# Optimization experiments

Measured on AMD Instinct MI355X. Metric: run time of the kernel, lower is better.

The kernel has to match this reference:

```python
import jax, jax.numpy as jnp
import numpy as np
from jax import lax

SEQ_LEN, PRED_LEN, D_MODEL, ENC_IN, D_FF, N_LAYERS, N_HEADS = 336, 192, 512, 64, 2048, 2, 8
NUM_STEPS, COF, MARK, B, LABEL_LEN = 2, 0.1, 4, 32, 48


def _pos_emb(T, D):
    pos = np.arange(T)[:, None].astype(np.float32)
    div = np.exp(np.arange(0, D, 2).astype(np.float32) * (-np.log(10000.0) / D))
    pe = np.zeros((T, D), np.float32)
    pe[:, 0::2] = np.sin(pos * div)
    pe[:, 1::2] = np.cos(pos * div)
    return jnp.asarray(pe)


def _layer_norm(x, g, b):
    mu = x.mean(-1, keepdims=True)
    var = ((x - mu) ** 2).mean(-1, keepdims=True)
    return (x - mu) * lax.rsqrt(var + 1e-5) * g + b


def _embed(x, mark, conv_w, tf_w):
    # TokenEmbedding: circular Conv1d(kernel=3, pad=1) over time, no bias
    T = x.shape[1]
    xp = jnp.concatenate([x[:, -1:], x, x[:, :1]], axis=1)  # circular pad
    tok = sum(jnp.einsum('btc,cd->btd', xp[:, k:k + T], conv_w[k]) for k in range(3))
    return tok + _pos_emb(T, conv_w.shape[2])[None] + mark @ tf_w


def _block(x, p):
    Wq, Wk, Wv, Wo, bq, bk, bv, bo, g1, be1, W1, b1, W2, b2, g2, be2 = p
    Bb, T, D = x.shape
    dh = D // N_HEADS
    q = (x @ Wq + bq).reshape(Bb, T, N_HEADS, dh)
    k = (x @ Wk + bk).reshape(Bb, T, N_HEADS, dh)
    v = (x @ Wv + bv).reshape(Bb, T, N_HEADS, dh)
    att = jax.nn.softmax(jnp.einsum('bthd,bshd->bhts', q, k) / jnp.sqrt(jnp.float32(dh)), axis=-1)
    o = jnp.einsum('bhts,bshd->bthd', att, v).reshape(Bb, T, D) @ Wo + bo
    x = _layer_norm(x + o, g1, be1)
    ff = jax.nn.relu(x @ W1 + b1) @ W2 + b2
    return _layer_norm(x + ff, g2, be2)


def _gru(x, h, wih, whh, bih, bhh):
    gi = x @ wih.T + bih
    gh = h @ whh.T + bhh
    ir, iz, inn = jnp.split(gi, 3, axis=-1)
    hr, hz, hn = jnp.split(gh, 3, axis=-1)
    r = jax.nn.sigmoid(ir + hr)
    z = jax.nn.sigmoid(iz + hz)
    n = jnp.tanh(inn + r * hn)
    return (1.0 - z) * n + z * h


def _langevin(corrupt, cond, hx0, gru_p, score_w, alpha):
    # per-step GRU + energy-gradient update (Langevin refinement)
    def step(hx, xc):
        xi, ci = xc  # [B,C] each
        def energy(ri):
            h = _gru(jnp.concatenate([ri, ci], -1), hx, *gru_p)
            return (h @ score_w).sum() * COF, h
        g, h_new = jax.grad(energy, has_aux=True)(xi)
        return h_new, xi - alpha * g
    _, out = lax.scan(step, hx0, (corrupt.transpose(1, 0, 2), cond.transpose(1, 0, 2)))
    return out.transpose(1, 0, 2)  # [B,P,C]


def _forward(x_enc, x_mark_enc, batch_y, batch_y_mark, hx_init, token_conv_w, timefeat_w,
             Wq, Wk, Wv, Wo, bq, bk, bv, bo, ln1_g, ln1_b, W1, b1, W2, b2, ln2_g, ln2_b,
             pl1_w, pl1_b, pl2_w, pl2_b, proj_w, proj_b,
             gru_wih, gru_whh, gru_bih, gru_bhh, score_w, alpha):
    means = lax.stop_gradient(x_enc.mean(1, keepdims=True))
    xe = x_enc - means
    stdev = jnp.sqrt(xe.var(1, keepdims=True) + 1e-5)  # not detached in torch code
    xe = xe / stdev
    # predict_linear1 over time axis: [B,T,C] -> [B,P,C]
    pre = jnp.einsum('btc,pt->bpc', xe, pl1_w) + pl1_b[None, :, None]
    ymark = batch_y_mark[:, -PRED_LEN:, :]
    gru_p = (gru_wih, gru_whh, gru_bih, gru_bhh)
    local_loss = jnp.float32(0.0)
    out_dn = None
    for s in range(NUM_STEPS):
        corrupt = lax.stop_gradient(pre)
        corrupt = jnp.einsum('bpc,qp->bqc', corrupt, pl2_w) + pl2_b[None, :, None]
        emb = _embed(corrupt, ymark, token_conv_w, timefeat_w)
        for l in range(N_LAYERS):
            emb = _block(emb, (Wq[l], Wk[l], Wv[l], Wo[l], bq[l], bk[l], bv[l], bo[l],
                               ln1_g[l], ln1_b[l], W1[l], b1[l], W2[l], b2[l], ln2_g[l], ln2_b[l]))
        cond = emb @ proj_w.T + proj_b
        out = _langevin(corrupt, cond, hx_init[s], gru_p, score_w, alpha)
        pre = out
        out_dn = out * stdev[:, 0, :][:, None, :] + means[:, 0, :][:, None, :]
        local_loss = local_loss + jnp.mean(jnp.abs(out_dn - batch_y[:, -PRED_LEN:, :]))
    return out_dn, local_loss


def setup_inputs() -> dict:
    key = jax.random.key(0)
    ks = iter(jax.random.split(key, 64))
    r = lambda shape, s=0.02: jax.random.normal(next(ks), shape, dtype=jnp.float32) * s
    inp = dict(
        x_enc=jax.random.normal(next(ks), (B, SEQ_LEN, ENC_IN), dtype=jnp.float32),
        x_mark_enc=jax.random.normal(next(ks), (B, SEQ_LEN, MARK), dtype=jnp.float32),
        batch_y=jax.random.normal(next(ks), (B, LABEL_LEN + PRED_LEN, ENC_IN), dtype=jnp.float32),
        batch_y_mark=jax.random.normal(next(ks), (B, LABEL_LEN + PRED_LEN, MARK), dtype=jnp.float32),
        hx_init=jax.random.normal(next(ks), (NUM_STEPS, B, D_MODEL), dtype=jnp.float32),
        token_conv_w=r((3, ENC_IN, D_MODEL)),
        timefeat_w=r((MARK, D_MODEL)),
        Wq=r((N_LAYERS, D_MODEL, D_MODEL)), Wk=r((N_LAYERS, D_MODEL, D_MODEL)),
        Wv=r((N_LAYERS, D_MODEL, D_MODEL)), Wo=r((N_LAYERS, D_MODEL, D_MODEL)),
        bq=jnp.zeros((N_LAYERS, D_MODEL)), bk=jnp.zeros((N_LAYERS, D_MODEL)),
        bv=jnp.zeros((N_LAYERS, D_MODEL)), bo=jnp.zeros((N_LAYERS, D_MODEL)),
        ln1_g=jnp.ones((N_LAYERS, D_MODEL)), ln1_b=jnp.zeros((N_LAYERS, D_MODEL)),
        W1=r((N_LAYERS, D_MODEL, D_FF)), b1=jnp.zeros((N_LAYERS, D_FF)),
        W2=r((N_LAYERS, D_FF, D_MODEL)), b2=jnp.zeros((N_LAYERS, D_MODEL)),
        ln2_g=jnp.ones((N_LAYERS, D_MODEL)), ln2_b=jnp.zeros((N_LAYERS, D_MODEL)),
        pl1_w=r((PRED_LEN, SEQ_LEN), 0.05), pl1_b=jnp.zeros((PRED_LEN,)),
        pl2_w=r((PRED_LEN, PRED_LEN), 0.05), pl2_b=jnp.zeros((PRED_LEN,)),
        proj_w=r((ENC_IN, D_MODEL)), proj_b=jnp.zeros((ENC_IN,)),
        gru_wih=r((3 * D_MODEL, 2 * ENC_IN), 0.04), gru_whh=r((3 * D_MODEL, D_MODEL), 0.04),
        gru_bih=jnp.zeros((3 * D_MODEL,)), gru_bhh=jnp.zeros((3 * D_MODEL,)),
        score_w=r((D_MODEL,), 0.04),
        alpha=jnp.array([0.1], dtype=jnp.float32),
    )
    return inp


def reference(x_enc, x_mark_enc, batch_y, batch_y_mark, hx_init, token_conv_w, timefeat_w,
              Wq, Wk, Wv, Wo, bq, bk, bv, bo, ln1_g, ln1_b, W1, b1, W2, b2, ln2_g, ln2_b,
              pl1_w, pl1_b, pl2_w, pl2_b, proj_w, proj_b,
              gru_wih, gru_whh, gru_bih, gru_bhh, score_w, alpha):
    out, loss = _forward(x_enc, x_mark_enc, batch_y, batch_y_mark, hx_init, token_conv_w, timefeat_w,
                         Wq, Wk, Wv, Wo, bq, bk, bv, bo, ln1_g, ln1_b, W1, b1, W2, b2, ln2_g, ln2_b,
                         pl1_w, pl1_b, pl2_w, pl2_b, proj_w, proj_b,
                         gru_wih, gru_whh, gru_bih, gru_bhh, score_w, alpha)
    return out[:, -PRED_LEN:, :], loss
```

## Files before the change

### kernel.cpp

```cpp
#include <hip/hip_runtime.h>
#include <math.h>

#define BATCH 32
#define TT    192
#define DM    512
#define CIN   64
#define SEQL  336
#define DFF   2048
#define NH    8
#define COF   0.1f
#define OUTN  (BATCH*TT*CIN)

typedef _Float16 h2_t __attribute__((ext_vector_type(2)));
union H2U { unsigned int u; h2_t h; };

typedef short bf16x8 __attribute__((ext_vector_type(8)));
typedef float f32x4 __attribute__((ext_vector_type(4)));
typedef unsigned int u32x4 __attribute__((ext_vector_type(4)));

__device__ __forceinline__ unsigned short f2bf(float v) {
  union { float f; unsigned int u; } a; a.f = v;
  unsigned int r = (a.u + 0x7fffu + ((a.u >> 16) & 1u)) >> 16;
  return (unsigned short)r;
}

__device__ __forceinline__ void gload16(const unsigned short* g, unsigned short* l) {
  __builtin_amdgcn_global_load_lds(
      (const __attribute__((address_space(1))) void*)g,
      (__attribute__((address_space(3))) void*)l, 16, 0, 0);
}

__device__ __forceinline__ int sd4(unsigned int a, unsigned int b, int c) {
#if __has_builtin(__builtin_amdgcn_sdot4)
  return __builtin_amdgcn_sdot4((int)a, (int)b, c, false);
#else
  c += (int)(signed char)(a & 0xff) * (int)(signed char)(b & 0xff);
  c += (int)(signed char)((a >> 8) & 0xff) * (int)(signed char)((b >> 8) & 0xff);
  c += (int)(signed char)((a >> 16) & 0xff) * (int)(signed char)((b >> 16) & 0xff);
  c += (int)(signed char)(a >> 24) * (int)(signed char)(b >> 24);
  return c;
#endif
}

__device__ __forceinline__ int sd16(u32x4 w, u32x4 h, int acc) {
  acc = sd4(w[0], h[0], acc); acc = sd4(w[1], h[1], acc);
  acc = sd4(w[2], h[2], acc); acc = sd4(w[3], h[3], acc);
  return acc;
}

__device__ __forceinline__ unsigned int packq4(const float* hp) {
  int a = (int)rintf(hp[0] * 15.875f); a = a < -127 ? -127 : (a > 127 ? 127 : a);
  int b = (int)rintf(hp[1] * 15.875f); b = b < -127 ? -127 : (b > 127 ? 127 : b);
  int c = (int)rintf(hp[2] * 15.875f); c = c < -127 ? -127 : (c > 127 ? 127 : c);
  int d = (int)rintf(hp[3] * 15.875f); d = d < -127 ? -127 : (d > 127 ? 127 : d);
  return (unsigned int)((a & 0xff) | ((b & 0xff) << 8) | ((c & 0xff) << 16) |
                        ((d & 0xff) << 24));
}


__global__ void zero_loss_kernel(float* loss) {
  if (threadIdx.x == 0) loss[0] = 0.f;
}

__global__ void zero_hqg_kernel(unsigned long long* p) {
  p[blockIdx.x * 256 + threadIdx.x] = 0ull;
}

__global__ void finalize_kernel(float* dout, const float* loss) {
  dout[OUTN] = loss[0] * (1.f / (float)OUTN);
}

__global__ void pe_table_kernel(float* __restrict__ peT) {
  int t = blockIdx.x, d = threadIdx.x;
  int i2 = (d >> 1) * 2;
  float freq = expf((float)i2 * (-9.210340371976184f / (float)DM));
  float ang = (float)t * freq;
  peT[(size_t)t * DM + d] = (d & 1) ? cosf(ang) : sinf(ang);
}

__global__ void stats_kernel(const float* __restrict__ x, float* __restrict__ means,
                             float* __restrict__ stdev) {
  int b = blockIdx.x, c = threadIdx.x;
  const float* xb = x + (size_t)b * SEQL * CIN + c;
  float s = 0.f;
  for (int t = 0; t < SEQL; t++) s += xb[t * CIN];
  float mu = s * (1.f / SEQL);
  float s2 = 0.f;
  for (int t = 0; t < SEQL; t++) { float d = xb[t * CIN] - mu; s2 += d * d; }
  means[b * CIN + c] = mu;
  stdev[b * CIN + c] = sqrtf(s2 * (1.f / SEQL) + 1e-5f);
}

__global__ void pl1_kernel(const float* __restrict__ x, const float* __restrict__ means,
                           const float* __restrict__ stdev, const float* __restrict__ w,
                           const float* __restrict__ bias, float* __restrict__ pre) {
  int p = blockIdx.x, b = blockIdx.y, c = threadIdx.x;
  float mu = means[b * CIN + c];
  float inv = 1.f / stdev[b * CIN + c];
  const float* xb = x + (size_t)b * SEQL * CIN + c;
  const float* wp = w + p * SEQL;
  float acc = 0.f;
  for (int t = 0; t < SEQL; t++) acc += (xb[t * CIN] - mu) * wp[t];
  pre[((size_t)b * TT + p) * CIN + c] = acc * inv + bias[p];
}

__global__ void pl2_kernel(const float* __restrict__ pre, const float* __restrict__ w,
                           const float* __restrict__ bias, float* __restrict__ out,
                           unsigned short* __restrict__ xc) {
  int q = blockIdx.x, b = blockIdx.y, c = threadIdx.x;
  const float* pb = pre + (size_t)b * TT * CIN + c;
  const float* wq = w + q * TT;
  float acc = 0.f;
  for (int p = 0; p < TT; p++) acc += pb[p * CIN] * wq[p];
  float val = acc + bias[q];
  size_t r = (size_t)b * TT + q;
  out[r * CIN + c] = val;
  xc[r * 128 + c] = f2bf(val);
}

__global__ void embed_kernel(const float* __restrict__ corrupt, const float* __restrict__ ymark,
                             const float* __restrict__ conv_w, const float* __restrict__ tf_w,
                             const float* __restrict__ peT, float* __restrict__ emb,
                             unsigned short* __restrict__ embB) {
  int t = blockIdx.x, b = blockIdx.y, d = threadIdx.x;
  __shared__ float xm[CIN], x0[CIN], xp[CIN], mk[4];
  int tm = (t + TT - 1) % TT, tp = (t + 1) % TT;
  if (d < CIN) {
    xm[d] = corrupt[((size_t)b * TT + tm) * CIN + d];
    x0[d] = corrupt[((size_t)b * TT + t) * CIN + d];
    xp[d] = corrupt[((size_t)b * TT + tp) * CIN + d];
  }
  if (d < 4) mk[d] = ymark[((size_t)b * 240 + 48 + t) * 4 + d];
  __syncthreads();
  float acc = 0.f;
  const float* w0 = conv_w + d;
  const float* w1 = conv_w + CIN * DM + d;
  const float* w2 = conv_w + 2 * CIN * DM + d;
  #pragma unroll 8
  for (int c = 0; c < CIN; c++)
    acc += xm[c] * w0[c * DM] + x0[c] * w1[c * DM] + xp[c] * w2[c * DM];
  float pe = peT[(size_t)t * DM + d];
  float mkacc = mk[0] * tf_w[d] + mk[1] * tf_w[DM + d] + mk[2] * tf_w[2 * DM + d] +
                mk[3] * tf_w[3 * DM + d];
  float val = acc + pe + mkacc;
  size_t o = ((size_t)b * TT + t) * DM + d;
  emb[o] = val;
  embB[o] = f2bf(val);
}

template <int TB, int RELU, int XC>
__global__ __launch_bounds__(256) void gemm_kernel(const float* __restrict__ A,
                                                   const float* __restrict__ B,
                                                   const float* __restrict__ bias,
                                                   float* __restrict__ C,
                                                   unsigned short* __restrict__ Cx,
                                                   int M, int N, int K) {
  __shared__ float As[16][68];
  __shared__ float Bs[16][68];
  int tid = threadIdx.x;
  int bn = blockIdx.x * 64, bm = blockIdx.y * 64;
  int tx = tid & 15, ty = tid >> 4;
  int row0 = ty * 4, col0 = tx * 4;
  float acc[4][4] = {};
  for (int k0 = 0; k0 < K; k0 += 16) {
    {
      int m = tid >> 2, kq = (tid & 3) << 2;
      float4 av = *(const float4*)&A[(size_t)(bm + m) * K + k0 + kq];
      As[kq + 0][m] = av.x; As[kq + 1][m] = av.y; As[kq + 2][m] = av.z; As[kq + 3][m] = av.w;
    }
    if (TB) {
      int n = tid >> 2, kq = (tid & 3) << 2;
      float4 bv = *(const float4*)&B[(size_t)(bn + n) * K + k0 + kq];
      Bs[kq + 0][n] = bv.x; Bs[kq + 1][n] = bv.y; Bs[kq + 2][n] = bv.z; Bs[kq + 3][n] = bv.w;
    } else {
      int kk = tid >> 4, nq = (tid & 15) << 2;
      float4 bv = *(const float4*)&B[(size_t)(k0 + kk) * N + bn + nq];
      *(float4*)&Bs[kk][nq] = bv;
    }
    __syncthreads();
    #pragma unroll
    for (int k = 0; k < 16; k++) {
      float4 a4 = *(const float4*)&As[k][row0];
      float4 b4 = *(const float4*)&Bs[k][col0];
      float a[4] = {a4.x, a4.y, a4.z, a4.w};
      float bb[4] = {b4.x, b4.y, b4.z, b4.w};
      #pragma unroll
      for (int i = 0; i < 4; i++)
        #pragma unroll
        for (int j = 0; j < 4; j++) acc[i][j] += a[i] * bb[j];
    }
    __syncthreads();
  }
  float bv[4] = {0.f, 0.f, 0.f, 0.f};
  if (bias) *(float4*)bv = *(const float4*)&bias[bn + col0];
  #pragma unroll
  for (int i = 0; i < 4; i++) {
    float ov[4];
    #pragma unroll
    for (int j = 0; j < 4; j++) {
      float v = acc[i][j] + bv[j];
      if (RELU) v = fmaxf(v, 0.f);
      ov[j] = v;
    }
    if (XC) {
      unsigned short xv[4];
      #pragma unroll
      for (int j = 0; j < 4; j++) xv[j] = f2bf(ov[j]);
      *(uint2*)&Cx[(size_t)(bm + row0 + i) * 128 + 64 + bn + col0] = *(uint2*)xv;
    } else {
      *(float4*)&C[(size_t)(bm + row0 + i) * N + bn + col0] = *(float4*)ov;
    }
  }
}

template <int RELU, int WF32, int WBF16>
__global__ __launch_bounds__(256) void gemm_bf16_kernel(
    const unsigned short* __restrict__ A, const unsigned short* __restrict__ Bt,
    const float* __restrict__ bias, float* __restrict__ C, unsigned short* __restrict__ Cb,
    int M, int N, int K) {
  __shared__ __align__(16) unsigned short As[128 * 32];
  __shared__ __align__(16) unsigned short Bs[128 * 32];
  int tid = threadIdx.x;
  int bm = blockIdx.y * 128, bn = blockIdx.x * 128;
  int wave = tid >> 6, lane = tid & 63;
  int wm = (wave >> 1) * 64, wn = (wave & 1) * 64;
  int r15 = lane & 15, q = lane >> 4;
  f32x4 acc[4][4] = {};
  int srow = wave * 32 + (lane >> 2);
  int scol = (lane & 3) * 8;
  for (int k0 = 0; k0 < K; k0 += 32) {
    gload16(&A[(size_t)(bm + srow) * K + k0 + scol], &As[(wave * 32) * 32]);
    gload16(&A[(size_t)(bm + srow + 16) * K + k0 + scol], &As[(wave * 32 + 16) * 32]);
    gload16(&Bt[(size_t)(bn + srow) * K + k0 + scol], &Bs[(wave * 32) * 32]);
    gload16(&Bt[(size_t)(bn + srow + 16) * K + k0 + scol], &Bs[(wave * 32 + 16) * 32]);
    __syncthreads();
    bf16x8 af[4], bfr[4];
    #pragma unroll
    for (int mi = 0; mi < 4; mi++)
      af[mi] = *(const bf16x8*)&As[(wm + mi * 16 + r15) * 32 + q * 8];
    #pragma unroll
    for (int ni = 0; ni < 4; ni++)
      bfr[ni] = *(const bf16x8*)&Bs[(wn + ni * 16 + r15) * 32 + q * 8];
    #pragma unroll
    for (int mi = 0; mi < 4; mi++)
      #pragma unroll
      for (int ni = 0; ni < 4; ni++)
        acc[mi][ni] =
            __builtin_amdgcn_mfma_f32_16x16x32_bf16(af[mi], bfr[ni], acc[mi][ni], 0, 0, 0);
    __syncthreads();
  }
  #pragma unroll
  for (int mi = 0; mi < 4; mi++) {
    #pragma unroll
    for (int ni = 0; ni < 4; ni++) {
      int col = bn + wn + ni * 16 + r15;
      float bv = bias ? bias[col] : 0.f;
      #pragma unroll
      for (int v = 0; v < 4; v++) {
        int row = bm + wm + mi * 16 + q * 4 + v;
        float val = acc[mi][ni][v] + bv;
        if (RELU) val = fmaxf(val, 0.f);
        if (WF32) C[(size_t)row * N + col] = val;
        if (WBF16) Cb[(size_t)row * N + col] = f2bf(val);
      }
    }
  }
}

__global__ __launch_bounds__(256) void axpy_partial_kernel(
    const unsigned short* __restrict__ A, const unsigned short* __restrict__ Bt,
    float* __restrict__ P, int M, int K) {
  __shared__ __align__(16) unsigned short As[128 * 32];
  __shared__ __align__(16) unsigned short Bs[128 * 32];
  int tid = threadIdx.x;
  int kq = blockIdx.x;
  int bm = blockIdx.y * 128;
  int wave = tid >> 6, lane = tid & 63;
  int wm = (wave >> 1) * 64, wn = (wave & 1) * 64;
  int r15 = lane & 15, q = lane >> 4;
  f32x4 acc[4][4] = {};
  int srow = wave * 32 + (lane >> 2);
  int scol = (lane & 3) * 8;
  int kbeg = kq * (K >> 2), kend = (kq + 1) * (K >> 2);
  for (int k0 = kbeg; k0 < kend; k0 += 32) {
    gload16(&A[(size_t)(bm + srow) * K + k0 + scol], &As[(wave * 32) * 32]);
    gload16(&A[(size_t)(bm + srow + 16) * K + k0 + scol], &As[(wave * 32 + 16) * 32]);
    gload16(&Bt[(size_t)srow * K + k0 + scol], &Bs[(wave * 32) * 32]);
    gload16(&Bt[(size_t)(srow + 16) * K + k0 + scol], &Bs[(wave * 32 + 16) * 32]);
    __syncthreads();
    bf16x8 af[4], bfr[4];
    #pragma unroll
    for (int mi = 0; mi < 4; mi++)
      af[mi] = *(const bf16x8*)&As[(wm + mi * 16 + r15) * 32 + q * 8];
    #pragma unroll
    for (int ni = 0; ni < 4; ni++)
      bfr[ni] = *(const bf16x8*)&Bs[(wn + ni * 16 + r15) * 32 + q * 8];
    #pragma unroll
    for (int mi = 0; mi < 4; mi++)
      #pragma unroll
      for (int ni = 0; ni < 4; ni++)
        acc[mi][ni] =
            __builtin_amdgcn_mfma_f32_16x16x32_bf16(af[mi], bfr[ni], acc[mi][ni], 0, 0, 0);
    __syncthreads();
  }
  #pragma unroll
  for (int mi = 0; mi < 4; mi++) {
    #pragma unroll
    for (int ni = 0; ni < 4; ni++) {
      int col = wn + ni * 16 + r15;
      if (col < 64) {
        #pragma unroll
        for (int v = 0; v < 4; v++) {
          int row = bm + wm + mi * 16 + q * 4 + v;
          P[(size_t)kq * OUTN + (size_t)row * 64 + col] = acc[mi][ni][v];
        }
      }
    }
  }
}

__global__ __launch_bounds__(256) void pack_transpose_bf16_kernel(
    const float* __restrict__ src, unsigned short* __restrict__ dst, int K, int N) {
  __shared__ unsigned short tile[64][65];
  int kb = blockIdx.x * 64, nb = blockIdx.y * 64;
  int tid = threadIdx.x;
  int tn = tid & 63, tk = tid >> 6;
  #pragma unroll
  for (int i = 0; i < 16; i++) {
    int k = tk + i * 4;
    tile[k][tn] = f2bf(src[(size_t)(kb + k) * N + nb + tn]);
  }
  __syncthreads();
  int tk2 = tid & 63, tn2 = tid >> 6;
  #pragma unroll
  for (int i = 0; i < 16; i++) {
    int n = tn2 + i * 4;
    dst[(size_t)(nb + n) * K + kb + tk2] = tile[tk2][n];
  }
}

__global__ void pack_bf16_kernel(const float* __restrict__ src, unsigned short* __restrict__ dst,
                                 int n) {
  int idx = blockIdx.x * 256 + threadIdx.x;
  if (idx < n) dst[idx] = f2bf(src[idx]);
}

__global__ void pack_wxproj_kernel(const float* __restrict__ wih,
                                   unsigned short* __restrict__ dst) {
  int idx = blockIdx.x * 256 + threadIdx.x;
  int k = idx % 1536, n = idx / 1536;
  float v = (n < 64) ? wih[(size_t)k * 128 + n] : 0.f;
  dst[idx] = f2bf(v);
}

__global__ void concat_qkv_bias_kernel(const float* __restrict__ bq, const float* __restrict__ bk,
                                       const float* __restrict__ bv, float* __restrict__ dst) {
  int l = blockIdx.y;
  int i = blockIdx.x * 256 + threadIdx.x;
  float v = (i < 512) ? bq[l * 512 + i]
                      : ((i < 1024) ? bk[l * 512 + i - 512] : bv[l * 512 + i - 1024]);
  dst[l * 1536 + i] = v;
}

__global__ __launch_bounds__(256) void attention_mfma_kernel(
    const unsigned short* __restrict__ qkv, unsigned short* __restrict__ attnO) {
  __shared__ __align__(16) unsigned short Ks[192 * 72];
  __shared__ __align__(16) unsigned short Vt[64 * 200];
  __shared__ __align__(16) float Ps[4][16 * 36];
  int h = blockIdx.x, b = blockIdx.y;
  int tid = threadIdx.x, wave = tid >> 6, lane = tid & 63;
  int m = lane & 15, q = lane >> 4;
  const unsigned short* Qg = qkv + (size_t)b * TT * 1536 + h * 64;
  const unsigned short* Kg = Qg + 512;
  const unsigned short* Vg = Qg + 1024;
  for (int idx = tid; idx < 192 * 8; idx += 256) {
    int s = idx >> 3, ch = (idx & 7) * 8;
    *(uint4*)&Ks[s * 72 + ch] = *(const uint4*)&Kg[(size_t)s * 1536 + ch];
  }
  for (int idx = tid; idx < 96 * 8; idx += 256) {
    int sp = idx >> 3, co = (idx & 7) * 8;
    uint4 v0 = *(const uint4*)&Vg[(size_t)(2 * sp) * 1536 + co];
    uint4 v1 = *(const uint4*)&Vg[(size_t)(2 * sp + 1) * 1536 + co];
    const unsigned short* e0 = (const unsigned short*)&v0;
    const unsigned short* e1 = (const unsigned short*)&v1;
    unsigned int* vtw = (unsigned int*)Vt;
    #pragma unroll
    for (int u = 0; u < 8; u++)
      vtw[(co + u) * 100 + sp] = (unsigned int)e0[u] | ((unsigned int)e1[u] << 16);
  }
  __syncthreads();
  float* ps = Ps[wave];
  for (int tile = wave; tile < 12; tile += 4) {
    int t0 = tile * 16;
    bf16x8 qf0 = *(const bf16x8*)&Qg[(size_t)(t0 + m) * 1536 + q * 8];
    bf16x8 qf1 = *(const bf16x8*)&Qg[(size_t)(t0 + m) * 1536 + 32 + q * 8];
    f32x4 S[12];
    #pragma unroll
    for (int nt = 0; nt < 12; nt++) {
      bf16x8 kf0 = *(const bf16x8*)&Ks[(nt * 16 + m) * 72 + q * 8];
      bf16x8 kf1 = *(const bf16x8*)&Ks[(nt * 16 + m) * 72 + 32 + q * 8];
      f32x4 a = {0.f, 0.f, 0.f, 0.f};
      a = __builtin_amdgcn_mfma_f32_16x16x32_bf16(qf0, kf0, a, 0, 0, 0);
      a = __builtin_amdgcn_mfma_f32_16x16x32_bf16(qf1, kf1, a, 0, 0, 0);
      S[nt] = a;
    }
    float mx[4] = {-1e30f, -1e30f, -1e30f, -1e30f};
    #pragma unroll
    for (int nt = 0; nt < 12; nt++)
      #pragma unroll
      for (int v = 0; v < 4; v++) {
        S[nt][v] *= 0.125f;
        mx[v] = fmaxf(mx[v], S[nt][v]);
      }
    #pragma unroll
    for (int d = 1; d < 16; d <<= 1) {
      #pragma unroll
      for (int v = 0; v < 4; v++) mx[v] = fmaxf(mx[v], __shfl_xor(mx[v], d));
    }
    float sm[4] = {0.f, 0.f, 0.f, 0.f};
    #pragma unroll
    for (int nt = 0; nt < 12; nt++)
      #pragma unroll
      for (int v = 0; v < 4; v++) {
        float e = __expf(S[nt][v] - mx[v]);
        S[nt][v] = e;
        sm[v] += e;
      }
    #pragma unroll
    for (int d = 1; d < 16; d <<= 1) {
      #pragma unroll
      for (int v = 0; v < 4; v++) sm[v] += __shfl_xor(sm[v], d);
    }
    float inv[4];
    #pragma unroll
    for (int v = 0; v < 4; v++) inv[v] = 1.f / sm[v];
    f32x4 o[4] = {};
    for (int kc = 0; kc < 6; kc++) {
      asm volatile("s_waitcnt lgkmcnt(0)" ::: "memory");
      #pragma unroll
      for (int half = 0; half < 2; half++) {
        int nt = 2 * kc + half;
        #pragma unroll
        for (int v = 0; v < 4; v++) ps[(q * 4 + v) * 36 + half * 16 + m] = S[nt][v];
      }
      asm volatile("s_waitcnt lgkmcnt(0)" ::: "memory");
      float4 p0 = *(const float4*)&ps[m * 36 + q * 8];
      float4 p1 = *(const float4*)&ps[m * 36 + q * 8 + 4];
      unsigned short tmp[8];
      tmp[0] = f2bf(p0.x); tmp[1] = f2bf(p0.y); tmp[2] = f2bf(p0.z); tmp[3] = f2bf(p0.w);
      tmp[4] = f2bf(p1.x); tmp[5] = f2bf(p1.y); tmp[6] = f2bf(p1.z); tmp[7] = f2bf(p1.w);
      bf16x8 pf = *(bf16x8*)tmp;
      #pragma unroll
      for (int nt2 = 0; nt2 < 4; nt2++) {
        bf16x8 vf = *(const bf16x8*)&Vt[(nt2 * 16 + m) * 200 + kc * 32 + q * 8];
        o[nt2] = __builtin_amdgcn_mfma_f32_16x16x32_bf16(pf, vf, o[nt2], 0, 0, 0);
      }
    }
    #pragma unroll
    for (int nt2 = 0; nt2 < 4; nt2++)
      #pragma unroll
      for (int v = 0; v < 4; v++) {
        size_t row = (size_t)b * TT + t0 + q * 4 + v;
        attnO[row * 512 + h * 64 + nt2 * 16 + m] = f2bf(o[nt2][v] * inv[v]);
      }
  }
}

__global__ __launch_bounds__(256) void ln_residual_kernel(float* __restrict__ x,
                                                          const float* __restrict__ res,
                                                          const float* __restrict__ g,
                                                          const float* __restrict__ b,
                                                          unsigned short* __restrict__ xb) {
  int row = blockIdx.x, tid = threadIdx.x;
  __shared__ float red[256];
  float* xr = x + (size_t)row * DM;
  const float* rr = res + (size_t)row * DM;
  float v0 = xr[tid] + rr[tid];
  float v1 = xr[tid + 256] + rr[tid + 256];
  red[tid] = v0 + v1;
  __syncthreads();
  if (tid < 128) red[tid] += red[tid + 128];
  __syncthreads();
  if (tid < 64) red[tid] += red[tid + 64];
  __syncthreads();
  float rv = red[tid & 63];
  #pragma unroll
  for (int s = 32; s > 0; s >>= 1) rv += __shfl_down(rv, s);
  float mu = __shfl(rv, 0) * (1.f / DM);
  __syncthreads();
  float d0 = v0 - mu, d1 = v1 - mu;
  red[tid] = d0 * d0 + d1 * d1;
  __syncthreads();
  if (tid < 128) red[tid] += red[tid + 128];
  __syncthreads();
  if (tid < 64) red[tid] += red[tid + 64];
  __syncthreads();
  rv = red[tid & 63];
  #pragma unroll
  for (int s = 32; s > 0; s >>= 1) rv += __shfl_down(rv, s);
  float rstd = rsqrtf(__shfl(rv, 0) * (1.f / DM) + 1e-5f);
  float o0 = d0 * rstd * g[tid] + b[tid];
  float o1 = d1 * rstd * g[tid + 256] + b[tid + 256];
  xr[tid] = o0;
  xr[tid + 256] = o1;
  xb[(size_t)row * DM + tid] = f2bf(o0);
  xb[(size_t)row * DM + tid + 256] = f2bf(o1);
}

__global__ void pack_whh_q8_kernel(const float* __restrict__ whh, signed char* __restrict__ whhJ,
                                   float* __restrict__ sws) {
  int row = blockIdx.x;
  int lane = threadIdx.x;
  const float* src = whh + (size_t)row * 512;
  float mx = 0.f;
  for (int k = lane; k < 512; k += 64) mx = fmaxf(mx, fabsf(src[k]));
  for (int off = 32; off > 0; off >>= 1) mx = fmaxf(mx, __shfl_xor(mx, off));
  float inv = (mx > 0.f) ? 127.f / mx : 0.f;
  if (lane == 0) sws[row] = (mx / 127.f) * (8.f / 127.f);
  int g = row >> 9, jj = row & 511;
  int quad = jj >> 7, jl = jj & 127;
  for (int k = lane; k < 512; k += 64) {
    int qv = (int)rintf(src[k] * inv);
    qv = qv < -127 ? -127 : (qv > 127 ? 127 : qv);
    int kh = k >> 6, u = (k >> 4) & 3, m = k & 15;
    whhJ[((size_t)(((quad * 128 + jl) * 8 + kh) * 4 + u) * 3 + g) * 16 + m] = (signed char)qv;
  }
}

__global__ __launch_bounds__(1024, 4) void langevin_scan_kernel(
    const float* __restrict__ gi_all, const float* __restrict__ hx0,
    const signed char* __restrict__ whhJ, const float* __restrict__ sws,
    const float* __restrict__ bhh, const float* __restrict__ score_w,
    unsigned short* __restrict__ dgiB, unsigned long long* __restrict__ hqg, int tagBase) {
  int b = blockIdx.x, quad = blockIdx.y;
  int tid = threadIdx.x;
  __shared__ __align__(16) unsigned int hqp[2][160];
  int jl = tid >> 3, kh = tid & 7;
  int j = quad * 128 + jl;
  bool act = (kh == 0);
  float bhr = 0.f, bhz = 0.f, bhn = 0.f, sw = 0.f, swr = 0.f, swz = 0.f, swn = 0.f, h = 0.f;
  if (act) {
    bhr = bhh[j]; bhz = bhh[512 + j]; bhn = bhh[1024 + j];
    sw = score_w[j] * COF;
    swr = sws[j]; swz = sws[512 + j]; swn = sws[1024 + j];
    h = hx0[(size_t)b * 512 + j];
  }
  if (tid < 128) {
    float4 hv = *(const float4*)&hx0[(size_t)b * 512 + tid * 4];
    float tmp[4] = {hv.x, hv.y, hv.z, hv.w};
    hqp[0][(tid >> 4) * 20 + (tid & 15)] = packq4(tmp);
  }
  const u32x4* wbase = (const u32x4*)whhJ + (size_t)((quad * 128 + jl) * 8 + kh) * 12;
  u32x4 wreg[12];
  #pragma unroll
  for (int i = 0; i < 12; i++) wreg[i] = wbase[i];
  #pragma unroll
  for (int i = 0; i < 12; i++) asm volatile("" : "+v"(wreg[i]));
  float gir = 0.f, giz = 0.f, gin = 0.f, gir1 = 0.f, giz1 = 0.f, gin1 = 0.f;
  if (act) {
    const float* g0 = &gi_all[(size_t)b * TT * 1536];
    gir = g0[j]; giz = g0[512 + j]; gin = g0[1024 + j];
    const float* g1 = g0 + 1536;
    gir1 = g1[j]; giz1 = g1[512 + j]; gin1 = g1[1024 + j];
  }
  __syncthreads();
  for (int t = 0; t < TT; t++) {
    int rb = t & 1;
    int ir = 0, iz = 0, in_ = 0;
    #pragma unroll
    for (int u = 0; u < 4; u++) {
      u32x4 hqv = *(const u32x4*)&hqp[rb][kh * 20 + u * 4];
      ir = sd16(wreg[u * 3 + 0], hqv, ir);
      iz = sd16(wreg[u * 3 + 1], hqv, iz);
      in_ = sd16(wreg[u * 3 + 2], hqv, in_);
    }
    #pragma unroll
    for (int d = 1; d < 8; d <<= 1) {
      ir += __shfl_xor(ir, d);
      iz += __shfl_xor(iz, d);
      in_ += __shfl_xor(in_, d);
    }
    int qv = 0;
    float r = 0.f, z = 0.f, n = 0.f, hnv = 0.f, hj = 0.f;
    if (act) {
      float gr = (float)ir * swr, gz = (float)iz * swz, gn2 = (float)in_ * swn;
      r = 1.f / (1.f + expf(-(gir + gr + bhr)));
      z = 1.f / (1.f + expf(-(giz + gz + bhz)));
      hnv = gn2 + bhn;
      n = tanhf(gin + r * hnv);
      hj = h;
      h = (1.f - z) * n + z * hj;
      int q = (int)rintf(h * 15.875f);
      qv = q < -127 ? -127 : (q > 127 ? 127 : q);
    }
    int l = tid & 63;
    int q1 = __shfl(qv, (l + 8) & 63);
    int q2 = __shfl(qv, (l + 16) & 63);
    int q3 = __shfl(qv, (l + 24) & 63);
    bool ex = (t + 1 < TT);
    int wb = (t + 1) & 1;
    unsigned tag = (unsigned)(tagBase + t + 1);
    if (ex && (tid & 31) == 0) {
      unsigned word = (unsigned)(qv & 0xff) | ((unsigned)(q1 & 0xff) << 8) |
                      ((unsigned)(q2 & 0xff) << 16) | ((unsigned)(q3 & 0xff) << 24);
      int w = quad * 32 + (tid >> 5);
      hqp[wb][(w >> 4) * 20 + (w & 15)] = word;
      __hip_atomic_store(&hqg[((size_t)wb * BATCH + b) * 128 + w],
                         ((unsigned long long)tag << 32) | (unsigned long long)word,
                         __ATOMIC_RELAXED, __HIP_MEMORY_SCOPE_AGENT);
    }
    float dg0 = 0.f, dg1 = 0.f, dg2 = 0.f;
    if (act) {
      float dinn = sw * (1.f - z) * (1.f - n * n);
      dg0 = dinn * hnv * r * (1.f - r);
      dg1 = sw * (hj - n) * z * (1.f - z);
      dg2 = dinn;
    }
    if (ex && kh == 1 && jl < 96) {
      int o = jl >> 5;
      int oq = (quad + 1 + o) & 3;
      int w = oq * 32 + (jl & 31);
      unsigned long long* p = &hqg[((size_t)wb * BATCH + b) * 128 + w];
      unsigned long long v = __hip_atomic_load(p, __ATOMIC_RELAXED, __HIP_MEMORY_SCOPE_AGENT);
      while ((unsigned)(v >> 32) != tag) {
        __builtin_amdgcn_s_sleep(1);
        v = __hip_atomic_load(p, __ATOMIC_RELAXED, __HIP_MEMORY_SCOPE_AGENT);
      }
      hqp[wb][(w >> 4) * 20 + (w & 15)] = (unsigned)v;
    }
    __builtin_amdgcn_sched_barrier(0);
    float girP = 0.f, gizP = 0.f, ginP = 0.f;
    if (act && t + 2 < TT) {
      const float* gp = &gi_all[((size_t)b * TT + t + 2) * 1536];
      girP = gp[j]; gizP = gp[512 + j]; ginP = gp[1024 + j];
    }
    if (act) {
      size_t drow = ((size_t)b * TT + t) * 1536;
      dgiB[drow + j] = f2bf(dg0);
      dgiB[drow + 512 + j] = f2bf(dg1);
      dgiB[drow + 1024 + j] = f2bf(dg2);
    }
    if (ex) __syncthreads();
    gir = gir1; giz = giz1; gin = gin1;
    gir1 = girP; giz1 = gizP; gin1 = ginP;
  }
}

__global__ __launch_bounds__(256) void denorm_loss_fused_kernel(
    const float* __restrict__ P, const float* __restrict__ R,
    const float* __restrict__ alphaPtr, const float* __restrict__ stdev,
    const float* __restrict__ means, const float* __restrict__ y,
    float* __restrict__ outn, float* __restrict__ dout, float* __restrict__ loss) {
  int idx = blockIdx.x * 256 + threadIdx.x;
  int tid = threadIdx.x;
  int c = idx & 63;
  int bt = idx >> 6;
  int t = bt % TT, b = bt / TT;
  float al = alphaPtr[0];
  float val = P[idx] + P[OUTN + idx] + P[2 * (size_t)OUTN + idx] + P[3 * (size_t)OUTN + idx];
  float on = R[idx] - al * val;
  outn[idx] = on;
  float od = on * stdev[b * CIN + c] + means[b * CIN + c];
  dout[idx] = od;
  float diff = fabsf(od - y[((size_t)b * 240 + 48 + t) * CIN + c]);
  __shared__ float red[256];
  red[tid] = diff;
  __syncthreads();
  if (tid < 128) red[tid] += red[tid + 128];
  __syncthreads();
  if (tid < 64) red[tid] += red[tid + 64];
  __syncthreads();
  if (tid < 64) {
    float rv = red[tid];
    #pragma unroll
    for (int s = 32; s > 0; s >>= 1) rv += __shfl_down(rv, s);
    if (tid == 0) atomicAdd(loss, rv);
  }
}

extern "C" void kernel_launch(void* const* d_in, const int* in_sizes, int n_in, void* d_out,
                              int out_size, void* d_ws, size_t ws_size, hipStream_t stream) {
  const float* x_enc = (const float*)d_in[0];
  const float* batch_y = (const float*)d_in[2];
  const float* y_mark = (const float*)d_in[3];
  const float* hx_init = (const float*)d_in[4];
  const float* conv_w = (const float*)d_in[5];
  const float* tf_w = (const float*)d_in[6];
  const float* Wq = (const float*)d_in[7];
  const float* Wk = (const float*)d_in[8];
  const float* Wv = (const float*)d_in[9];
  const float* Wo = (const float*)d_in[10];
  const float* bq = (const float*)d_in[11];
  const float* bk = (const float*)d_in[12];
  const float* bv = (const float*)d_in[13];
  const float* bo = (const float*)d_in[14];
  const float* ln1_g = (const float*)d_in[15];
  const float* ln1_b = (const float*)d_in[16];
  const float* W1 = (const float*)d_in[17];
  const float* b1 = (const float*)d_in[18];
  const float* W2 = (const float*)d_in[19];
  const float* b2 = (const float*)d_in[20];
  const float* ln2_g = (const float*)d_in[21];
  const float* ln2_b = (const float*)d_in[22];
  const float* pl1_w = (const float*)d_in[23];
  const float* pl1_b = (const float*)d_in[24];
  const float* pl2_w = (const float*)d_in[25];
  const float* pl2_b = (const float*)d_in[26];
  const float* proj_w = (const float*)d_in[27];
  const float* proj_b = (const float*)d_in[28];
  const float* gru_wih = (const float*)d_in[29];
  const float* gru_whh = (const float*)d_in[30];
  const float* gru_bih = (const float*)d_in[31];
  const float* gru_bhh = (const float*)d_in[32];
  const float* score_w = (const float*)d_in[33];
  const float* alpha = (const float*)d_in[34];
  float* dout = (float*)d_out;

  float* W = (float*)d_ws;
  size_t off = 0;
  float* means = W + off;   off += 2048;
  float* stdev = W + off;   off += 2048;
  float* lossacc = W + off; off += 64;
  float* preA = W + off;    off += (size_t)OUTN;
  float* outA = W + off;    off += (size_t)OUTN;
  float* outB = W + off;    off += (size_t)OUTN;
  float* corrupt = W + off; off += (size_t)OUTN;
  float* peT = W + off;     off += (size_t)TT * DM;
  float* axp = W + off;     off += (size_t)4 * OUTN;
  signed char* whhJ = (signed char*)(W + off); off += 786432 / 4;
  float* sws = W + off;     off += 1536;
  unsigned long long* hqg = (unsigned long long*)(W + off); off += 2 * BATCH * 128 * 2;
  float* emb = W + off;     off += (size_t)BATCH * TT * DM;
  float* Kb = W + off;      off += (size_t)BATCH * TT * DM;
  float* gi_all = W + off;  off += (size_t)BATCH * TT * 1536;
  unsigned short* embB = (unsigned short*)(W + off);  off += (size_t)BATCH * TT * DM / 2;
  unsigned short* qkvB = (unsigned short*)(W + off);  off += (size_t)BATCH * TT * 1536 / 2;
  unsigned short* attnOB = (unsigned short*)(W + off); off += (size_t)BATCH * TT * DM / 2;
  unsigned short* FFbB = (unsigned short*)(W + off);  off += (size_t)BATCH * TT * DFF / 2;
  unsigned short* xcatB = (unsigned short*)(W + off); off += (size_t)BATCH * TT * 128 / 2;
  float* bqkv = W + off;    off += 2 * 1536;
  unsigned short* WxProjB = (unsigned short*)(W + off); off += (size_t)128 * 1536 / 2;
  unsigned short* wT = (unsigned short*)(W + off);
  const size_t SQ = (size_t)DM * DM;
  const size_t SFF = (size_t)DM * DFF;
  const size_t LAYER = 4 * SQ + 2 * SFF;
  unsigned short* wihB = wT + 2 * LAYER;
  off += (2 * LAYER + (size_t)1536 * 128) / 2 + 64;
  unsigned short* dgiB = qkvB;

  const int M = BATCH * TT;

  zero_loss_kernel<<<1, 64, 0, stream>>>(lossacc);
  zero_hqg_kernel<<<32, 256, 0, stream>>>(hqg);
  pe_table_kernel<<<TT, DM, 0, stream>>>(peT);
  stats_kernel<<<BATCH, 64, 0, stream>>>(x_enc, means, stdev);
  pl1_kernel<<<dim3(TT, BATCH), 64, 0, stream>>>(x_enc, means, stdev, pl1_w, pl1_b, preA);
  pack_whh_q8_kernel<<<1536, 64, 0, stream>>>(gru_whh, whhJ, sws);
  pack_wxproj_kernel<<<(128 * 1536) / 256, 256, 0, stream>>>(gru_wih, WxProjB);
  concat_qkv_bias_kernel<<<dim3(6, 2), 256, 0, stream>>>(bq, bk, bv, bqkv);
  for (int l = 0; l < 2; l++) {
    unsigned short* base = wT + (size_t)l * LAYER;
    pack_transpose_bf16_kernel<<<dim3(8, 8), 256, 0, stream>>>(Wq + (size_t)l * SQ, base, DM, DM);
    pack_transpose_bf16_kernel<<<dim3(8, 8), 256, 0, stream>>>(Wk + (size_t)l * SQ, base + SQ, DM, DM);
    pack_transpose_bf16_kernel<<<dim3(8, 8), 256, 0, stream>>>(Wv + (size_t)l * SQ, base + 2 * SQ, DM, DM);
    pack_transpose_bf16_kernel<<<dim3(8, 8), 256, 0, stream>>>(Wo + (size_t)l * SQ, base + 3 * SQ, DM, DM);
    pack_transpose_bf16_kernel<<<dim3(8, 32), 256, 0, stream>>>(W1 + (size_t)l * SFF, base + 4 * SQ, DM, DFF);
    pack_transpose_bf16_kernel<<<dim3(32, 8), 256, 0, stream>>>(W2 + (size_t)l * SFF, base + 4 * SQ + SFF, DFF, DM);
  }
  pack_bf16_kernel<<<(1536 * 128) / 256, 256, 0, stream>>>(gru_wih, wihB, 1536 * 128);

  const float* pre = preA;
  float* outs[2] = {outA, outB};
  for (int s = 0; s < 2; s++) {
    pl2_kernel<<<dim3(TT, BATCH), 64, 0, stream>>>(pre, pl2_w, pl2_b, corrupt, xcatB);
    embed_kernel<<<dim3(TT, BATCH), DM, 0, stream>>>(corrupt, y_mark, conv_w, tf_w, peT, emb,
                                                     embB);
    for (int l = 0; l < 2; l++) {
      unsigned short* base = wT + (size_t)l * LAYER;
      gemm_bf16_kernel<0, 0, 1><<<dim3(1536 / 128, M / 128), 256, 0, stream>>>(
          embB, base, bqkv + l * 1536, nullptr, qkvB, M, 1536, DM);
      attention_mfma_kernel<<<dim3(NH, BATCH), 256, 0, stream>>>(qkvB, attnOB);
      gemm_bf16_kernel<0, 1, 0><<<dim3(DM / 128, M / 128), 256, 0, stream>>>(
          attnOB, base + 3 * SQ, bo + l * DM, Kb, nullptr, M, DM, DM);
      ln_residual_kernel<<<M, 256, 0, stream>>>(emb, Kb, ln1_g + l * DM, ln1_b + l * DM, embB);
      gemm_bf16_kernel<1, 0, 1><<<dim3(DFF / 128, M / 128), 256, 0, stream>>>(
          embB, base + 4 * SQ, b1 + l * DFF, nullptr, FFbB, M, DFF, DM);
      gemm_bf16_kernel<0, 1, 0><<<dim3(DM / 128, M / 128), 256, 0, stream>>>(
          FFbB, base + 4 * SQ + SFF, b2 + l * DM, Kb, nullptr, M, DM, DFF);
      ln_residual_kernel<<<M, 256, 0, stream>>>(emb, Kb, ln2_g + l * DM, ln2_b + l * DM, embB);
    }
    gemm_kernel<1, 0, 1><<<dim3(CIN / 64, M / 64), 256, 0, stream>>>(
        emb, proj_w, proj_b, nullptr, xcatB, M, CIN, DM);
    gemm_bf16_kernel<0, 1, 0><<<dim3(1536 / 128, M / 128), 256, 0, stream>>>(
        xcatB, wihB, gru_bih, gi_all, nullptr, M, 1536, 128);
    langevin_scan_kernel<<<dim3(BATCH, 4), 1024, 0, stream>>>(
        gi_all, hx_init + (size_t)s * BATCH * DM, whhJ, sws, gru_bhh, score_w, dgiB, hqg,
        s * TT);
    axpy_partial_kernel<<<dim3(4, M / 128), 256, 0, stream>>>(dgiB, WxProjB, axp, M, 1536);
    denorm_loss_fused_kernel<<<OUTN / 256, 256, 0, stream>>>(
        axp, corrupt, alpha, stdev, means, batch_y, outs[s], dout, lossacc);
    pre = outs[s];
  }
  finalize_kernel<<<1, 1, 0, stream>>>(dout, lossacc);
}
```

Measured before the change: 2.360 ms.

## Recast token and time-feature embedding as a tiled GEMM over an im2col buffer

Replaces the per-(t,b) embed kernel, which rereads the conv and time-feature weights from global memory for every token, with an im2col-style build of a padded [M,208] input matrix followed by the existing tiled fp32 GEMM against a stacked weight matrix. The positional encoding is added and the bf16 copy written in the GEMM epilogue. This adds an extra kernel launch and a round trip of the Xp buffer through memory, but gives shared-memory weight reuse across rows. The embedding stage is a small part of the total runtime.

```diff
diff --git a/kernel.cpp b/kernel.cpp
--- a/kernel.cpp
+++ b/kernel.cpp
@@ -10,6 +10,7 @@
 #define NH    8
 #define COF   0.1f
 #define OUTN  (BATCH*TT*CIN)
+#define KEMB  208
 
 typedef _Float16 h2_t __attribute__((ext_vector_type(2)));
 union H2U { unsigned int u; h2_t h; };
@@ -76,6 +77,38 @@
   float freq = expf((float)i2 * (-9.210340371976184f / (float)DM));
   float ang = (float)t * freq;
   peT[(size_t)t * DM + d] = (d & 1) ? cosf(ang) : sinf(ang);
+}
+
+__global__ void build_wemb_kernel(const float* __restrict__ conv_w,
+                                  const float* __restrict__ tf_w, float* __restrict__ Wemb) {
+  int idx = blockIdx.x * 256 + threadIdx.x;
+  int n = idx % DM, k = idx / DM;
+  float v = 0.f;
+  if (k < 192) v = conv_w[(size_t)k * DM + n];
+  else if (k < 196) v = tf_w[(size_t)(k - 192) * DM + n];
+  Wemb[idx] = v;
+}
+
+__global__ void build_xp_kernel(const float* __restrict__ corrupt,
+                                const float* __restrict__ ymark, float* __restrict__ Xp) {
+  int idx = blockIdx.x * 256 + threadIdx.x;
+  int col = idx % KEMB, row = idx / KEMB;
+  int b = row / TT, t = row % TT;
+  float v;
+  if (col < 64) {
+    int tm = (t + TT - 1) % TT;
+    v = corrupt[((size_t)b * TT + tm) * CIN + col];
+  } else if (col < 128) {
+    v = corrupt[((size_t)b * TT + t) * CIN + (col - 64)];
+  } else if (col < 192) {
+    int tp = (t + 1) % TT;
+    v = corrupt[((size_t)b * TT + tp) * CIN + (col - 128)];
+  } else if (col < 196) {
+    v = ymark[((size_t)b * 240 + 48 + t) * 4 + (col - 192)];
+  } else {
+    v = 0.f;
+  }
+  Xp[idx] = v;
 }
 
 __global__ void stats_kernel(const float* __restrict__ x, float* __restrict__ means,
@@ -118,42 +151,14 @@
   xc[r * 128 + c] = f2bf(val);
 }
 
-__global__ void embed_kernel(const float* __restrict__ corrupt, const float* __restrict__ ymark,
-                             const float* __restrict__ conv_w, const float* __restrict__ tf_w,
-                             const float* __restrict__ peT, float* __restrict__ emb,
-                             unsigned short* __restrict__ embB) {
-  int t = blockIdx.x, b = blockIdx.y, d = threadIdx.x;
-  __shared__ float xm[CIN], x0[CIN], xp[CIN], mk[4];
-  int tm = (t + TT - 1) % TT, tp = (t + 1) % TT;
-  if (d < CIN) {
-    xm[d] = corrupt[((size_t)b * TT + tm) * CIN + d];
-    x0[d] = corrupt[((size_t)b * TT + t) * CIN + d];
-    xp[d] = corrupt[((size_t)b * TT + tp) * CIN + d];
-  }
-  if (d < 4) mk[d] = ymark[((size_t)b * 240 + 48 + t) * 4 + d];
-  __syncthreads();
-  float acc = 0.f;
-  const float* w0 = conv_w + d;
-  const float* w1 = conv_w + CIN * DM + d;
-  const float* w2 = conv_w + 2 * CIN * DM + d;
-  #pragma unroll 8
-  for (int c = 0; c < CIN; c++)
-    acc += xm[c] * w0[c * DM] + x0[c] * w1[c * DM] + xp[c] * w2[c * DM];
-  float pe = peT[(size_t)t * DM + d];
-  float mkacc = mk[0] * tf_w[d] + mk[1] * tf_w[DM + d] + mk[2] * tf_w[2 * DM + d] +
-                mk[3] * tf_w[3 * DM + d];
-  float val = acc + pe + mkacc;
-  size_t o = ((size_t)b * TT + t) * DM + d;
-  emb[o] = val;
-  embB[o] = f2bf(val);
-}
-
-template <int TB, int RELU, int XC>
+template <int TB, int RELU, int XC, int EMB>
 __global__ __launch_bounds__(256) void gemm_kernel(const float* __restrict__ A,
                                                    const float* __restrict__ B,
                                                    const float* __restrict__ bias,
                                                    float* __restrict__ C,
                                                    unsigned short* __restrict__ Cx,
+                                                   const float* __restrict__ PE,
+                                                   unsigned short* __restrict__ Cb2,
                                                    int M, int N, int K) {
   __shared__ float As[16][68];
   __shared__ float Bs[16][68];
@@ -195,10 +200,17 @@
   if (bias) *(float4*)bv = *(const float4*)&bias[bn + col0];
   #pragma unroll
   for (int i = 0; i < 4; i++) {
+    int row = bm + row0 + i;
+    float pe[4] = {0.f, 0.f, 0.f, 0.f};
+    if (EMB) {
+      int t = row % TT;
+      *(float4*)pe = *(const float4*)&PE[(size_t)t * DM + bn + col0];
+    }
     float ov[4];
     #pragma unroll
     for (int j = 0; j < 4; j++) {
       float v = acc[i][j] + bv[j];
+      if (EMB) v += pe[j];
       if (RELU) v = fmaxf(v, 0.f);
       ov[j] = v;
     }
@@ -206,9 +218,15 @@
       unsigned short xv[4];
       #pragma unroll
       for (int j = 0; j < 4; j++) xv[j] = f2bf(ov[j]);
-      *(uint2*)&Cx[(size_t)(bm + row0 + i) * 128 + 64 + bn + col0] = *(uint2*)xv;
+      *(uint2*)&Cx[(size_t)row * 128 + 64 + bn + col0] = *(uint2*)xv;
     } else {
-      *(float4*)&C[(size_t)(bm + row0 + i) * N + bn + col0] = *(float4*)ov;
+      *(float4*)&C[(size_t)row * N + bn + col0] = *(float4*)ov;
+      if (EMB) {
+        unsigned short xv[4];
+        #pragma unroll
+        for (int j = 0; j < 4; j++) xv[j] = f2bf(ov[j]);
+        *(uint2*)&Cb2[(size_t)row * N + bn + col0] = *(uint2*)xv;
+      }
     }
   }
 }
@@ -726,7 +744,9 @@
   float* outB = W + off;    off += (size_t)OUTN;
   float* corrupt = W + off; off += (size_t)OUTN;
   float* peT = W + off;     off += (size_t)TT * DM;
+  float* Wemb = W + off;    off += (size_t)KEMB * DM;
   float* axp = W + off;     off += (size_t)4 * OUTN;
+  float* Xp = axp;
   signed char* whhJ = (signed char*)(W + off); off += 786432 / 4;
   float* sws = W + off;     off += 1536;
   unsigned long long* hqg = (unsigned long long*)(W + off); off += 2 * BATCH * 128 * 2;
@@ -753,6 +773,7 @@
   zero_loss_kernel<<<1, 64, 0, stream>>>(lossacc);
   zero_hqg_kernel<<<32, 256, 0, stream>>>(hqg);
   pe_table_kernel<<<TT, DM, 0, stream>>>(peT);
+  build_wemb_kernel<<<(KEMB * DM) / 256, 256, 0, stream>>>(conv_w, tf_w, Wemb);
   stats_kernel<<<BATCH, 64, 0, stream>>>(x_enc, means, stdev);
   pl1_kernel<<<dim3(TT, BATCH), 64, 0, stream>>>(x_enc, means, stdev, pl1_w, pl1_b, preA);
   pack_whh_q8_kernel<<<1536, 64, 0, stream>>>(gru_whh, whhJ, sws);
@@ -773,8 +794,9 @@
   float* outs[2] = {outA, outB};
   for (int s = 0; s < 2; s++) {
     pl2_kernel<<<dim3(TT, BATCH), 64, 0, stream>>>(pre, pl2_w, pl2_b, corrupt, xcatB);
-    embed_kernel<<<dim3(TT, BATCH), DM, 0, stream>>>(corrupt, y_mark, conv_w, tf_w, peT, emb,
-                                                     embB);
+    build_xp_kernel<<<(M * KEMB) / 256, 256, 0, stream>>>(corrupt, y_mark, Xp);
+    gemm_kernel<0, 0, 0, 1><<<dim3(DM / 64, M / 64), 256, 0, stream>>>(
+        Xp, Wemb, nullptr, emb, nullptr, peT, embB, M, DM, KEMB);
     for (int l = 0; l < 2; l++) {
       unsigned short* base = wT + (size_t)l * LAYER;
       gemm_bf16_kernel<0, 0, 1><<<dim3(1536 / 128, M / 128), 256, 0, stream>>>(
@@ -789,8 +811,8 @@
           FFbB, base + 4 * SQ + SFF, b2 + l * DM, Kb, nullptr, M, DM, DFF);
       ln_residual_kernel<<<M, 256, 0, stream>>>(emb, Kb, ln2_g + l * DM, ln2_b + l * DM, embB);
     }
-    gemm_kernel<1, 0, 1><<<dim3(CIN / 64, M / 64), 256, 0, stream>>>(
-        emb, proj_w, proj_b, nullptr, xcatB, M, CIN, DM);
+    gemm_kernel<1, 0, 1, 0><<<dim3(CIN / 64, M / 64), 256, 0, stream>>>(
+        emb, proj_w, proj_b, nullptr, xcatB, nullptr, nullptr, M, CIN, DM);
     gemm_bf16_kernel<0, 1, 0><<<dim3(1536 / 128, M / 128), 256, 0, stream>>>(
         xcatB, wihB, gru_bih, gi_all, nullptr, M, 1536, 128);
     langevin_scan_kernel<<<dim3(BATCH, 4), 1024, 0, stream>>>(
```

New measurement: 2.227 ms. 5.7% less time.
